# Optimization experiments

Measured on AMD Instinct MI355X. Metric: run time of the kernel, lower is better.

## Reference

```python
import jax, jax.numpy as jnp
import numpy as np

D_MODEL, D_STATE, D_CONV, EXPAND = 512, 16, 4, 2
D_INNER = D_MODEL * EXPAND
BATCH, LENGTH = 2, 2048

def setup_inputs() -> dict:
    key = jax.random.key(0)
    ks = jax.random.split(key, 12)
    def lecun(k, shape, fan_in):
        return jax.random.normal(k, shape, jnp.float32) * (1.0 / np.sqrt(fan_in))
    x = jax.random.normal(ks[0], (BATCH, LENGTH, D_MODEL), jnp.float32)
    w_in = lecun(ks[1], (D_MODEL, 2 * D_INNER), D_MODEL)
    conv_k = lecun(ks[2], (D_CONV, D_INNER, D_INNER), D_CONV * D_INNER)  # (L_k, in, out)
    conv_b = jnp.zeros((D_INNER,), jnp.float32)
    w_delta = lecun(ks[3], (D_INNER, D_INNER), D_INNER)
    b_delta = jnp.zeros((D_INNER,), jnp.float32)
    w_B = lecun(ks[4], (D_INNER, D_STATE), D_INNER)
    b_B = jnp.zeros((D_STATE,), jnp.float32)
    w_C = lecun(ks[5], (D_INNER, D_STATE), D_INNER)
    b_C = jnp.zeros((D_STATE,), jnp.float32)
    A = lecun(ks[6], (D_INNER, D_STATE), D_INNER)  # dead param in original (deltaA unused)
    w_out = lecun(ks[7], (D_INNER, D_MODEL), D_INNER)
    return {"x": x, "w_in": w_in, "conv_k": conv_k, "conv_b": conv_b,
            "w_delta": w_delta, "b_delta": b_delta, "w_B": w_B, "b_B": b_B,
            "w_C": w_C, "b_C": b_C, "A": A, "w_out": w_out}

def reference(x, w_in, conv_k, conv_b, w_delta, b_delta, w_B, b_B, w_C, b_C, A, w_out):
    batch, length, _ = x.shape
    # input projection and gate split
    x_proj = x @ w_in                                   # (B, L, 2*d_inner)
    x_z, z = jnp.split(x_proj, 2, axis=-1)              # each (B, L, d_inner)
    # depthwise-style SAME conv over L (flax nn.Conv: full conv, kernel (Lk, in, out))
    x_conv = jax.lax.conv_general_dilated(
        x_z, conv_k, window_strides=(1,), padding='SAME',
        dimension_numbers=('NLC', 'LIO', 'NLC')) + conv_b
    x_conv = jax.nn.silu(x_conv)                        # (B, L, d_inner)
    delta = jax.nn.softplus(x_conv @ w_delta + b_delta)  # (B, L, d_inner)
    Bm = x_conv @ w_B + b_B                             # (B, L, d_state)
    Cm = x_conv @ w_C + b_C                             # (B, L, d_state)
    # NOTE: original computes deltaA = exp(delta * -exp(A)) but never uses it (dead code).
    deltaB_x = delta[..., None] * Bm[..., None, :] * x_conv[..., :, None]  # (B,L,d_inner,d_state)
    decay = jnp.cumprod(jnp.full((length,), 0.95, x.dtype))  # 0.95^(t+1)
    hidden = jnp.cumsum(deltaB_x * decay[None, :, None, None], axis=1)
    y = jnp.einsum('blns,bls->bln', hidden, Cm)         # (B, L, d_inner)
    y = y * jax.nn.silu(z)
    return y @ w_out                                    # (B, L, d_model)
```

## Files before the change

kernel.cpp:

```cpp
#include <hip/hip_runtime.h>
#include <hip/hip_bf16.h>
#include <math.h>

#define DMODEL 512
#define DINNER 1024
#define DSTATE 16
#define SEQLEN 2048
#define NTOK   4096
#define CHUNK  64
#define NCHUNK (SEQLEN / CHUNK)

typedef __bf16 bf16x8 __attribute__((ext_vector_type(8)));
typedef float  f32x4  __attribute__((ext_vector_type(4)));

__device__ __forceinline__ float silu_f(float x) {
    return x / (1.0f + __expf(-x));
}

__device__ __forceinline__ int swz(int r, int s) {
    return r * 64 + ((s ^ (r & 7)) << 3);
}

__device__ __forceinline__ void gload16(const void* g, void* l) {
    __builtin_amdgcn_global_load_lds(
        (const __attribute__((address_space(1))) void*)g,
        (__attribute__((address_space(3))) void*)l, 16, 0, 0);
}

__device__ __forceinline__ void cvt4(const float* src, __hip_bfloat16* dst) {
    float4 v = *reinterpret_cast<const float4*>(src);
    __hip_bfloat16 tmp[4] = {__float2bfloat16(v.x), __float2bfloat16(v.y),
                             __float2bfloat16(v.z), __float2bfloat16(v.w)};
    *reinterpret_cast<ushort4*>(dst) = *reinterpret_cast<const ushort4*>(tmp);
}

template<int MODE, int TBM, int TBN>
__global__ __launch_bounds__(256)
void mgemm(const __hip_bfloat16* __restrict__ A, int lda,
           const __hip_bfloat16* __restrict__ WT, int ldw,
           float* __restrict__ C0, __hip_bfloat16* __restrict__ Cb,
           __hip_bfloat16* __restrict__ Czb, int ldc,
           int K, const float* __restrict__ bias,
           const __hip_bfloat16* __restrict__ xc,
           const __hip_bfloat16* __restrict__ WT2, int ldw2,
           const __hip_bfloat16* __restrict__ zpage,
           const float* __restrict__ bB, const float* __restrict__ bC,
           float* __restrict__ BmO, float* __restrict__ CmO)
{
    constexpr int MI = TBM / 32;
    constexpr int MJ = TBN / 32;
    __shared__ __align__(16) __hip_bfloat16 As[TBM * 64];
    __shared__ __align__(16) __hip_bfloat16 Bs[TBN * 64];

    const int nb  = gridDim.x * gridDim.y;
    const int lin = blockIdx.y * gridDim.x + blockIdx.x;
    const int cpx = nb >> 3;
    const int sl  = (lin & 7) * cpx + (lin >> 3);
    const int bm  = (sl / gridDim.x) * TBM;
    const int bn  = (sl % gridDim.x) * TBN;

    if (MODE == 4) { A += blockIdx.z * 1024; Cb += blockIdx.z * 512; }

    const bool zblk = (MODE == 0) && (bn >= DINNER);
    const int  bnb  = zblk ? (bn - DINNER) : bn;
    const __hip_bfloat16* Wp = zblk ? WT2 : WT;
    const int  ldwp = zblk ? ldw2 : ldw;
    const int  Keff = zblk ? DMODEL : K;

    const int tid  = threadIdx.x;
    const int wid  = tid >> 6, lane = tid & 63;
    const int wr   = (wid >> 1) * (TBM / 2), wc = (wid & 1) * (TBN / 2);
    const int llo  = lane & 15, lhi = lane >> 4;

    f32x4 acc[MI][MJ] = {};

    const int srow0 = wid * 8 + (lane >> 3);
    const int sphys = lane & 7;

    auto stage_tile = [&](int k0) {
#pragma unroll
        for (int q = 0; q < MI; ++q) {
            int row  = q * 32 + srow0;
            int sdat = sphys ^ (row & 7);
            const __hip_bfloat16* srcA;
            if (MODE == 0 && !zblk) {
                int kid = k0 >> 9;
                int gr  = bm + row;
                int l2  = (gr & (SEQLEN - 1)) + kid - 1;
                srcA = ((unsigned)l2 < (unsigned)SEQLEN)
                     ? A + (size_t)(gr + kid - 1) * lda + (k0 & 511) + sdat * 8
                     : zpage;
            } else {
                srcA = A + (size_t)(bm + row) * lda + k0 + sdat * 8;
            }
            gload16(srcA, &As[q * 2048 + wid * 512]);
        }
#pragma unroll
        for (int q = 0; q < MJ; ++q) {
            int row  = q * 32 + srow0;
            int sdat = sphys ^ (row & 7);
            gload16(Wp + (size_t)(bnb + row) * ldwp + k0 + sdat * 8,
                    &Bs[q * 2048 + wid * 512]);
        }
    };

    const int NT = Keff / 64;
    for (int t = 0; t < NT; ++t) {
        stage_tile(t * 64);
        __syncthreads();
#pragma unroll
        for (int kk = 0; kk < 2; ++kk) {
            bf16x8 af[MI], bv[MJ];
#pragma unroll
            for (int i = 0; i < MI; ++i)
                af[i] = *reinterpret_cast<const bf16x8*>(&As[swz(wr + i * 16 + llo, kk * 4 + lhi)]);
#pragma unroll
            for (int j = 0; j < MJ; ++j)
                bv[j] = *reinterpret_cast<const bf16x8*>(&Bs[swz(wc + j * 16 + llo, kk * 4 + lhi)]);
#pragma unroll
            for (int i = 0; i < MI; ++i)
#pragma unroll
                for (int j = 0; j < MJ; ++j)
                    acc[i][j] = __builtin_amdgcn_mfma_f32_16x16x32_bf16(af[i], bv[j], acc[i][j], 0, 0, 0);
        }
        __syncthreads();
    }

#pragma unroll
    for (int i = 0; i < MI; ++i) {
#pragma unroll
        for (int q = 0; q < 4; ++q) {
            int m = bm + wr + i * 16 + lhi * 4 + q;
            float dec = 1.0f;
            if (MODE == 2)
                dec = __expf((float)((m & (SEQLEN - 1)) + 1) * -0.051293294f);
#pragma unroll
            for (int j = 0; j < MJ; ++j) {
                int nrel = wc + j * 16 + llo;
                int n = bn + nrel;
                float v = acc[i][j][q];
                if (MODE == 0) {
                    if (!zblk) {
                        v = silu_f(v + bias[n]);
                        Cb[(size_t)m * DINNER + n] = __float2bfloat16(v);
                    } else {
                        Czb[(size_t)m * DINNER + bnb + nrel] = __float2bfloat16(v);
                    }
                } else if (MODE == 2) {
                    if (n < DINNER) {
                        float d  = v + bias[n];
                        float sp = fmaxf(d, 0.f) + log1pf(__expf(-fabsf(d)));
                        float xcv = __bfloat162float(xc[(size_t)m * DINNER + n]);
                        Cb[(size_t)m * DINNER + n] = __float2bfloat16(sp * xcv * dec);
                    } else {
                        int col = n - DINNER;
                        if (col < 16)
                            BmO[(size_t)m * DSTATE + col] = v + bB[col];
                        else if (col < 32)
                            CmO[(size_t)m * DSTATE + (col - 16)] = v + bC[col - 16];
                    }
                } else if (MODE == 4) {
                    Cb[(size_t)m * ldc + n] = __float2bfloat16(v);
                } else {
                    C0[(size_t)m * ldc + n] = v;
                }
            }
        }
    }
}

__global__ __launch_bounds__(256)
void prep_k(const float* __restrict__ x, const float* __restrict__ w_in,
            const float* __restrict__ conv_k, const float* __restrict__ w_del,
            const float* __restrict__ w_B, const float* __restrict__ w_C,
            const float* __restrict__ w_out,
            __hip_bfloat16* __restrict__ xb, __hip_bfloat16* __restrict__ W1b,
            __hip_bfloat16* __restrict__ w2T, __hip_bfloat16* __restrict__ convT,
            __hip_bfloat16* __restrict__ wdelT, __hip_bfloat16* __restrict__ woutT,
            __hip_bfloat16* __restrict__ zpage)
{
    __shared__ float t[32][33];
    const int b = blockIdx.x, tid = threadIdx.x;
    if (b < 2048) {
        int idx = b * 256 + tid;
        int r = idx >> 7, c = (idx & 127) * 4;
        cvt4(x + (size_t)r * DMODEL + c, xb + (size_t)r * DMODEL + c);
    } else if (b < 2560) {
        int idx = (b - 2048) * 256 + tid;
        int r = idx >> 8, c = (idx & 255) * 4;
        cvt4(w_in + (size_t)r * (2 * DINNER) + c, W1b + (size_t)r * DINNER + c);
    } else if (b < 8704) {
        const float* in; __hip_bfloat16* outp; int R, ldin, ntx, local;
        if (b < 3072)      { local = b - 2560; in = w_in + DINNER; outp = w2T;   R = 512;  ldin = 2048; ntx = 32; }
        else if (b < 7168) { local = b - 3072; in = conv_k;        outp = convT; R = 4096; ldin = 1024; ntx = 32; }
        else if (b < 8192) { local = b - 7168; in = w_del;         outp = wdelT; R = 1024; ldin = 1024; ntx = 32; }
        else               { local = b - 8192; in = w_out;         outp = woutT; R = 1024; ldin = 512;  ntx = 16; }
        int bx = (local % ntx) * 32, by = (local / ntx) * 32;
        int tx = tid & 31, ty = tid >> 5;
#pragma unroll
        for (int q = 0; q < 4; ++q)
            t[ty + q * 8][tx] = in[(size_t)(by + ty + q * 8) * ldin + bx + tx];
        __syncthreads();
#pragma unroll
        for (int q = 0; q < 4; ++q)
            outp[(size_t)(bx + ty + q * 8) * R + by + tx] = __float2bfloat16(t[tx][ty + q * 8]);
    } else if (b < 8832) {
        int idx = (b - 8704) * 256 + tid;
        int sel = idx >> 14;
        int rem = idx & 16383;
        int s = rem >> 10, k = rem & 1023;
        const float* src = sel ? w_C : w_B;
        wdelT[(size_t)(1024 + sel * 16 + s) * DINNER + k] =
            __float2bfloat16(src[(size_t)k * DSTATE + s]);
    } else {
        int local = b - 8832;
        ushort4 zero = {0, 0, 0, 0};
        if (local < 8) {
            int idx = local * 256 + tid;
            *reinterpret_cast<ushort4*>(&zpage[idx * 4]) = zero;
        } else {
            int idx = (local - 8) * 256 + tid;
            *reinterpret_cast<ushort4*>(&wdelT[(size_t)1056 * DINNER + idx * 4]) = zero;
        }
    }
}

__global__ __launch_bounds__(256)
void chunkS_k(const __hip_bfloat16* __restrict__ wb, const float* __restrict__ Bm,
              float* __restrict__ S)
{
    constexpr int LDW = 72;
    __shared__ __align__(16) __hip_bfloat16 wT[128 * LDW];
    __shared__ __align__(16) __hip_bfloat16 bT[16 * 80];
    const int bc = blockIdx.x, n0 = blockIdx.y * 128, t0 = bc * CHUNK;
    const int tid = threadIdx.x;
#pragma unroll
    for (int q = 0; q < 8; ++q) {
        int idx = tid + q * 256;
        int t = idx >> 5, n4 = (idx & 31) * 4;
        int key = ((n4 >> 2) & 7) << 3;
        int tx = t ^ key;
        ushort4 v = *reinterpret_cast<const ushort4*>(
            &wb[(size_t)(t0 + t) * DINNER + n0 + n4]);
        wT[(n4 + 0) * LDW + tx] = *(const __hip_bfloat16*)&v.x;
        wT[(n4 + 1) * LDW + tx] = *(const __hip_bfloat16*)&v.y;
        wT[(n4 + 2) * LDW + tx] = *(const __hip_bfloat16*)&v.z;
        wT[(n4 + 3) * LDW + tx] = *(const __hip_bfloat16*)&v.w;
    }
#pragma unroll
    for (int q = 0; q < 4; ++q) {
        int idx = tid + q * 256;
        int t = idx >> 4, s = idx & 15;
        bT[s * 80 + t] = __float2bfloat16(Bm[(size_t)(t0 + t) * DSTATE + s]);
    }
    __syncthreads();
    const int wid = tid >> 6, lane = tid & 63;
    const int llo = lane & 15, lhi = lane >> 4;
    f32x4 acc[2] = {};
#pragma unroll
    for (int kk = 0; kk < 2; ++kk) {
        bf16x8 bv = *reinterpret_cast<const bf16x8*>(&bT[llo * 80 + kk * 32 + lhi * 8]);
#pragma unroll
        for (int i = 0; i < 2; ++i) {
            int r = wid * 32 + i * 16 + llo;
            int kbase = (kk * 32 + lhi * 8) ^ (((r >> 2) & 7) << 3);
            bf16x8 af = *reinterpret_cast<const bf16x8*>(&wT[r * LDW + kbase]);
            acc[i] = __builtin_amdgcn_mfma_f32_16x16x32_bf16(af, bv, acc[i], 0, 0, 0);
        }
    }
#pragma unroll
    for (int i = 0; i < 2; ++i)
#pragma unroll
        for (int q = 0; q < 4; ++q) {
            int n = wid * 32 + i * 16 + lhi * 4 + q;
            S[((size_t)bc * DINNER + n0 + n) * DSTATE + llo] = acc[i][q];
        }
}

__global__ __launch_bounds__(256)
void hpre_k(const float* __restrict__ S, __hip_bfloat16* __restrict__ Hb)
{
    int idx = blockIdx.x * 256 + threadIdx.x;
    int b  = idx >> 14;
    int ns = idx & 16383;
    float acc = 0.f;
    for (int c = 0; c < NCHUNK; ++c) {
        size_t off = ((size_t)(b * NCHUNK + c)) * (DINNER * DSTATE) + ns;
        Hb[off] = __float2bfloat16(acc);
        acc += S[off];
    }
}

__global__ __launch_bounds__(256)
void intra_k(const __hip_bfloat16* __restrict__ wb,
             const float* __restrict__ Bm, const float* __restrict__ Cm,
             const __hip_bfloat16* __restrict__ Hb,
             const __hip_bfloat16* __restrict__ zb,
             __hip_bfloat16* __restrict__ gb)
{
    constexpr int LDP  = 104;
    constexpr int LDC  = 40;
    __shared__ __align__(16) __hip_bfloat16 csb[64 * LDC];
    __shared__ __align__(16) __hip_bfloat16 bsb[64 * LDC];
    __shared__ __align__(16) __hip_bfloat16 Pb [64 * LDP];
    __shared__ __align__(16) __hip_bfloat16 Wb [64 * LDP];

    const int bc = blockIdx.x;
    const int n0 = blockIdx.y * 64;
    const int t0 = bc * CHUNK;
    const int tid = threadIdx.x;
    const int wid = tid >> 6, lane = tid & 63;
    const int llo = lane & 15, lhi = lane >> 4;
    const int wr = (wid >> 1) * 32, wc = (wid & 1) * 32;
    const __hip_bfloat16 z16 = __float2bfloat16(0.f);

#pragma unroll
    for (int q = 0; q < 4; ++q) {
        int idx = tid + q * 256;
        int j = idx >> 4, s = idx & 15;
        __hip_bfloat16 cb = __float2bfloat16(Cm[(size_t)(t0 + j) * DSTATE + s]);
        csb[j * LDC + s]      = cb;
        csb[j * LDC + 16 + s] = z16;
        bsb[j * LDC + s]      = __float2bfloat16(Bm[(size_t)(t0 + j) * DSTATE + s]);
        bsb[j * LDC + 16 + s] = z16;
        Pb[j * LDP + 64 + s]  = cb;
        Pb[j * LDP + 80 + s]  = z16;
        Wb[j * LDP + 64 + s]  = Hb[((size_t)bc * DINNER + n0 + j) * DSTATE + s];
        Wb[j * LDP + 80 + s]  = z16;
    }
#pragma unroll
    for (int q = 0; q < 4; ++q) {
        int c = tid + q * 256;
        int t = c >> 4, c4 = (c & 15) * 4;
        ushort4 v = *reinterpret_cast<const ushort4*>(
            &wb[(size_t)(t0 + t) * DINNER + n0 + c4]);
        Wb[(c4 + 0) * LDP + t] = *(const __hip_bfloat16*)&v.x;
        Wb[(c4 + 1) * LDP + t] = *(const __hip_bfloat16*)&v.y;
        Wb[(c4 + 2) * LDP + t] = *(const __hip_bfloat16*)&v.z;
        Wb[(c4 + 3) * LDP + t] = *(const __hip_bfloat16*)&v.w;
    }
    __syncthreads();

    {
        f32x4 pacc[2][2] = {};
        bf16x8 ap[2], bp[2];
#pragma unroll
        for (int i = 0; i < 2; ++i)
            ap[i] = *reinterpret_cast<const bf16x8*>(&csb[(wr + i * 16 + llo) * LDC + lhi * 8]);
#pragma unroll
        for (int j = 0; j < 2; ++j)
            bp[j] = *reinterpret_cast<const bf16x8*>(&bsb[(wc + j * 16 + llo) * LDC + lhi * 8]);
#pragma unroll
        for (int i = 0; i < 2; ++i)
#pragma unroll
            for (int j = 0; j < 2; ++j)
                pacc[i][j] = __builtin_amdgcn_mfma_f32_16x16x32_bf16(ap[i], bp[j], pacc[i][j], 0, 0, 0);
#pragma unroll
        for (int i = 0; i < 2; ++i)
#pragma unroll
            for (int q = 0; q < 4; ++q) {
                int l = wr + i * 16 + lhi * 4 + q;
#pragma unroll
                for (int j = 0; j < 2; ++j) {
                    int t = wc + j * 16 + llo;
                    float pv = (t <= l) ? pacc[i][j][q] : 0.f;
                    Pb[l * LDP + t] = __float2bfloat16(pv);
                }
            }
    }
    __syncthreads();

    f32x4 yacc[2][2] = {};
#pragma unroll
    for (int k0 = 0; k0 < 3; ++k0) {
        bf16x8 af[2], bv[2];
#pragma unroll
        for (int i = 0; i < 2; ++i)
            af[i] = *reinterpret_cast<const bf16x8*>(&Pb[(wr + i * 16 + llo) * LDP + k0 * 32 + lhi * 8]);
#pragma unroll
        for (int j = 0; j < 2; ++j)
            bv[j] = *reinterpret_cast<const bf16x8*>(&Wb[(wc + j * 16 + llo) * LDP + k0 * 32 + lhi * 8]);
#pragma unroll
        for (int i = 0; i < 2; ++i)
#pragma unroll
            for (int j = 0; j < 2; ++j)
                yacc[i][j] = __builtin_amdgcn_mfma_f32_16x16x32_bf16(af[i], bv[j], yacc[i][j], 0, 0, 0);
    }

#pragma unroll
    for (int i = 0; i < 2; ++i)
#pragma unroll
        for (int q = 0; q < 4; ++q) {
            int l = wr + i * 16 + lhi * 4 + q;
            int token = t0 + l;
#pragma unroll
            for (int j = 0; j < 2; ++j) {
                int n = wc + j * 16 + llo;
                float z = __bfloat162float(zb[(size_t)token * DINNER + n0 + n]);
                gb[(size_t)token * DINNER + n0 + n] =
                    __float2bfloat16(yacc[i][j][q] * silu_f(z));
            }
        }
}

extern "C" void kernel_launch(void* const* d_in, const int* in_sizes, int n_in,
                              void* d_out, int out_size, void* d_ws, size_t ws_size,
                              hipStream_t stream) {
    const float* x      = (const float*)d_in[0];
    const float* w_in   = (const float*)d_in[1];
    const float* conv_k = (const float*)d_in[2];
    const float* conv_b = (const float*)d_in[3];
    const float* w_del  = (const float*)d_in[4];
    const float* b_del  = (const float*)d_in[5];
    const float* w_B    = (const float*)d_in[6];
    const float* b_B    = (const float*)d_in[7];
    const float* w_C    = (const float*)d_in[8];
    const float* b_C    = (const float*)d_in[9];
    const float* w_out  = (const float*)d_in[11];
    float* out = (float*)d_out;

    float* Bm    = (float*)d_ws;
    float* Cm    = Bm + (size_t)NTOK * DSTATE;
    float* S     = Cm + (size_t)NTOK * DSTATE;
    __hip_bfloat16* Hb    = (__hip_bfloat16*)(S + (size_t)2 * NCHUNK * DINNER * DSTATE);
    __hip_bfloat16* xb    = Hb    + (size_t)2 * NCHUNK * DINNER * DSTATE;
    __hip_bfloat16* xcb   = xb    + (size_t)NTOK * DMODEL;
    __hip_bfloat16* zb    = xcb   + (size_t)NTOK * DINNER;
    __hip_bfloat16* gb    = zb    + (size_t)NTOK * DINNER;
    __hip_bfloat16* wbufb = gb    + (size_t)NTOK * DINNER;
    __hip_bfloat16* W1b   = wbufb + (size_t)NTOK * DINNER;
    __hip_bfloat16* w2T   = W1b   + (size_t)DMODEL * DINNER;
    __hip_bfloat16* convT = w2T   + (size_t)DINNER * DMODEL;
    __hip_bfloat16* wdelT = convT + (size_t)4 * DINNER * DINNER;
    __hip_bfloat16* woutT = wdelT + (size_t)1088 * DINNER;
    __hip_bfloat16* FT    = woutT + (size_t)DINNER * DMODEL;
    __hip_bfloat16* zpage = FT    + (size_t)DINNER * 2048;

    prep_k<<<8872, 256, 0, stream>>>(x, w_in, conv_k, w_del, w_B, w_C, w_out,
                                     xb, W1b, w2T, convT, wdelT, woutT, zpage);

    mgemm<4, 64, 64><<<dim3(DMODEL / 64, DINNER / 64, 4), 256, 0, stream>>>(
        convT, 4 * DINNER, W1b, DINNER, nullptr, FT, nullptr, 4 * DMODEL, DINNER,
        nullptr, nullptr, nullptr, 0, zpage, nullptr, nullptr, nullptr, nullptr);
    mgemm<0, 128, 64><<<dim3(2 * DINNER / 64, NTOK / 128), 256, 0, stream>>>(
        xb, DMODEL, FT, 4 * DMODEL, nullptr, xcb, zb, DINNER, 4 * DMODEL,
        conv_b, nullptr, w2T, DMODEL, zpage, nullptr, nullptr, nullptr, nullptr);
    mgemm<2, 128, 64><<<dim3(1088 / 64, NTOK / 128), 256, 0, stream>>>(
        xcb, DINNER, wdelT, DINNER, nullptr, wbufb, nullptr, DINNER, DINNER,
        b_del, xcb, nullptr, 0, zpage, b_B, b_C, Bm, Cm);
    chunkS_k<<<dim3(2 * NCHUNK, DINNER / 128), 256, 0, stream>>>(wbufb, Bm, S);
    hpre_k<<<dim3(2 * DINNER * DSTATE / 256), 256, 0, stream>>>(S, Hb);
    intra_k<<<dim3(2 * NCHUNK, DINNER / 64), 256, 0, stream>>>(wbufb, Bm, Cm, Hb, zb, gb);
    mgemm<3, 64, 64><<<dim3(DMODEL / 64, NTOK / 64), 256, 0, stream>>>(
        gb, DINNER, woutT, DINNER, out, nullptr, nullptr, DMODEL, DINNER,
        nullptr, nullptr, nullptr, 0, zpage, nullptr, nullptr, nullptr, nullptr);
}
```

Before: 134.9 us.

## Split conv GEMM along K into two partial products and combine in separate kernel

The fused input-projection/conv GEMM now splits its K=2048 reduction for the x_conv columns into two halves computed by separate blocks, giving a 48-wide grid instead of 32. Each half writes a bf16 partial, and a new elementwise kernel sums them, adds the conv bias and applies SiLU. This spreads the long-K blocks across more workgroups so the GPU stays fuller. In exchange it adds an extra kernel launch, extra global traffic for the two partial buffers, and an additional bf16 rounding of each partial before the sum.

```diff
diff --git a/kernel.cpp b/kernel.cpp
--- a/kernel.cpp
+++ b/kernel.cpp
@@ -45,7 +45,8 @@
            const __hip_bfloat16* __restrict__ WT2, int ldw2,
            const __hip_bfloat16* __restrict__ zpage,
            const float* __restrict__ bB, const float* __restrict__ bC,
-           float* __restrict__ BmO, float* __restrict__ CmO)
+           float* __restrict__ BmO, float* __restrict__ CmO,
+           __hip_bfloat16* __restrict__ Pb1)
 {
     constexpr int MI = TBM / 32;
     constexpr int MJ = TBN / 32;
@@ -61,11 +62,13 @@
 
     if (MODE == 4) { A += blockIdx.z * 1024; Cb += blockIdx.z * 512; }
 
-    const bool zblk = (MODE == 0) && (bn >= DINNER);
-    const int  bnb  = zblk ? (bn - DINNER) : bn;
+    const int  xsel = (MODE == 0) ? (bn >> 10) : 0;
+    const bool zblk = (MODE == 0) && (xsel == 2);
+    const int  bnb  = (MODE == 0) ? (bn & 1023) : bn;
     const __hip_bfloat16* Wp = zblk ? WT2 : WT;
     const int  ldwp = zblk ? ldw2 : ldw;
-    const int  Keff = zblk ? DMODEL : K;
+    const int  Keff = (MODE == 0 && zblk) ? DMODEL : K;
+    const int  koff = (MODE == 0 && xsel == 1) ? 1024 : 0;
 
     const int tid  = threadIdx.x;
     const int wid  = tid >> 6, lane = tid & 63;
@@ -84,11 +87,12 @@
             int sdat = sphys ^ (row & 7);
             const __hip_bfloat16* srcA;
             if (MODE == 0 && !zblk) {
-                int kid = k0 >> 9;
+                int kg  = koff + k0;
+                int kid = kg >> 9;
                 int gr  = bm + row;
                 int l2  = (gr & (SEQLEN - 1)) + kid - 1;
                 srcA = ((unsigned)l2 < (unsigned)SEQLEN)
-                     ? A + (size_t)(gr + kid - 1) * lda + (k0 & 511) + sdat * 8
+                     ? A + (size_t)(gr + kid - 1) * lda + (kg & 511) + sdat * 8
                      : zpage;
             } else {
                 srcA = A + (size_t)(bm + row) * lda + k0 + sdat * 8;
@@ -99,7 +103,7 @@
         for (int q = 0; q < MJ; ++q) {
             int row  = q * 32 + srow0;
             int sdat = sphys ^ (row & 7);
-            gload16(Wp + (size_t)(bnb + row) * ldwp + k0 + sdat * 8,
+            gload16(Wp + (size_t)(bnb + row) * ldwp + koff + k0 + sdat * 8,
                     &Bs[q * 2048 + wid * 512]);
         }
     };
@@ -140,11 +144,12 @@
                 int n = bn + nrel;
                 float v = acc[i][j][q];
                 if (MODE == 0) {
-                    if (!zblk) {
-                        v = silu_f(v + bias[n]);
-                        Cb[(size_t)m * DINNER + n] = __float2bfloat16(v);
+                    int col = bnb + nrel;
+                    if (zblk) {
+                        Czb[(size_t)m * DINNER + col] = __float2bfloat16(v);
                     } else {
-                        Czb[(size_t)m * DINNER + bnb + nrel] = __float2bfloat16(v);
+                        __hip_bfloat16* P = xsel ? Pb1 : Cb;
+                        P[(size_t)m * DINNER + col] = __float2bfloat16(v);
                     }
                 } else if (MODE == 2) {
                     if (n < DINNER) {
@@ -170,6 +175,27 @@
 }
 
 __global__ __launch_bounds__(256)
+void combine_k(const __hip_bfloat16* __restrict__ P0,
+               const __hip_bfloat16* __restrict__ P1,
+               const float* __restrict__ bias,
+               __hip_bfloat16* __restrict__ xcb)
+{
+    int idx = blockIdx.x * 256 + threadIdx.x;
+    size_t off = (size_t)idx * 4;
+    int n = (int)(off & 1023);
+    ushort4 a = *reinterpret_cast<const ushort4*>(&P0[off]);
+    ushort4 b = *reinterpret_cast<const ushort4*>(&P1[off]);
+    __hip_bfloat16 o[4];
+#pragma unroll
+    for (int j = 0; j < 4; ++j) {
+        float va = __bfloat162float(((const __hip_bfloat16*)&a)[j]);
+        float vb = __bfloat162float(((const __hip_bfloat16*)&b)[j]);
+        o[j] = __float2bfloat16(silu_f(va + vb + bias[n + j]));
+    }
+    *reinterpret_cast<ushort4*>(&xcb[off]) = *reinterpret_cast<const ushort4*>(o);
+}
+
+__global__ __launch_bounds__(256)
 void prep_k(const float* __restrict__ x, const float* __restrict__ w_in,
             const float* __restrict__ conv_k, const float* __restrict__ w_del,
             const float* __restrict__ w_B, const float* __restrict__ w_C,
@@ -435,23 +461,26 @@
     __hip_bfloat16* woutT = wdelT + (size_t)1088 * DINNER;
     __hip_bfloat16* FT    = woutT + (size_t)DINNER * DMODEL;
     __hip_bfloat16* zpage = FT    + (size_t)DINNER * 2048;
+    __hip_bfloat16* P0    = zpage + 8192;
+    __hip_bfloat16* P1    = P0    + (size_t)NTOK * DINNER;
 
     prep_k<<<8872, 256, 0, stream>>>(x, w_in, conv_k, w_del, w_B, w_C, w_out,
                                      xb, W1b, w2T, convT, wdelT, woutT, zpage);
 
     mgemm<4, 64, 64><<<dim3(DMODEL / 64, DINNER / 64, 4), 256, 0, stream>>>(
         convT, 4 * DINNER, W1b, DINNER, nullptr, FT, nullptr, 4 * DMODEL, DINNER,
-        nullptr, nullptr, nullptr, 0, zpage, nullptr, nullptr, nullptr, nullptr);
-    mgemm<0, 128, 64><<<dim3(2 * DINNER / 64, NTOK / 128), 256, 0, stream>>>(
-        xb, DMODEL, FT, 4 * DMODEL, nullptr, xcb, zb, DINNER, 4 * DMODEL,
-        conv_b, nullptr, w2T, DMODEL, zpage, nullptr, nullptr, nullptr, nullptr);
+        nullptr, nullptr, nullptr, 0, zpage, nullptr, nullptr, nullptr, nullptr, nullptr);
+    mgemm<0, 128, 64><<<dim3(48, NTOK / 128), 256, 0, stream>>>(
+        xb, DMODEL, FT, 4 * DMODEL, nullptr, P0, zb, DINNER, 1024,
+        nullptr, nullptr, w2T, DMODEL, zpage, nullptr, nullptr, nullptr, nullptr, P1);
+    combine_k<<<NTOK * DINNER / 1024, 256, 0, stream>>>(P0, P1, conv_b, xcb);
     mgemm<2, 128, 64><<<dim3(1088 / 64, NTOK / 128), 256, 0, stream>>>(
         xcb, DINNER, wdelT, DINNER, nullptr, wbufb, nullptr, DINNER, DINNER,
-        b_del, xcb, nullptr, 0, zpage, b_B, b_C, Bm, Cm);
+        b_del, xcb, nullptr, 0, zpage, b_B, b_C, Bm, Cm, nullptr);
     chunkS_k<<<dim3(2 * NCHUNK, DINNER / 128), 256, 0, stream>>>(wbufb, Bm, S);
     hpre_k<<<dim3(2 * DINNER * DSTATE / 256), 256, 0, stream>>>(S, Hb);
     intra_k<<<dim3(2 * NCHUNK, DINNER / 64), 256, 0, stream>>>(wbufb, Bm, Cm, Hb, zb, gb);
     mgemm<3, 64, 64><<<dim3(DMODEL / 64, NTOK / 64), 256, 0, stream>>>(
         gb, DINNER, woutT, DINNER, out, nullptr, nullptr, DMODEL, DINNER,
-        nullptr, nullptr, nullptr, 0, zpage, nullptr, nullptr, nullptr, nullptr);
-}
+        nullptr, nullptr, nullptr, 0, zpage, nullptr, nullptr, nullptr, nullptr, nullptr);
+}
```

After: 132.4 us. About the same (-1.9%).
